# Kernel tuning notes

Measured on AMD Instinct MI355X. Metric: run time of the kernel, lower is better.

The kernel has to match this reference:

```python
import jax, jax.numpy as jnp
import numpy as np

B, H, W, C = 32, 64, 64, 256


def setup_inputs() -> dict:
    key = jax.random.key(0)
    kq, kk, kv = jax.random.split(key, 3)
    query = jax.random.normal(kq, (B, H, W, C), dtype=jnp.float32)
    keys = jax.random.normal(kk, (B, H, W, C), dtype=jnp.float32)
    values = jax.random.normal(kv, (B, H, W, C), dtype=jnp.float32)
    return {"query": query, "keys": keys, "values": values}


def reference(query, keys, values):
    # A[b,q,k] = sum_{h,w} query[b,h,w,q] * keys[b,h,w,k]
    scores = jnp.einsum("bhwq,bhwk->bqk", query, keys)
    attn = jax.nn.softmax(scores, axis=-1)  # softmax over keys axis
    # out[b,q,h,w] = sum_k attn[b,q,k] * values[b,h,w,k]
    out = jnp.einsum("bqk,bhwk->bqhw", attn, values)
    return out
```

## Files before the change

kernel.cpp:

```cpp
#include <hip/hip_runtime.h>
#include <hip/hip_bf16.h>

#define B_  32
#define HW_ 4096
#define C_  256

using bf16x8 = __attribute__((ext_vector_type(8))) short;
using f32x4  = __attribute__((ext_vector_type(4))) float;
using u32x4  = __attribute__((ext_vector_type(4))) uint;

__device__ __forceinline__ ushort f2bf_rn(float x) {
    uint u = __builtin_bit_cast(uint, x);
    u += 0x7FFFu + ((u >> 16) & 1u);
    return (ushort)(u >> 16);
}
__device__ __forceinline__ uint pk_bf2(float a, float b) {
    return ((uint)f2bf_rn(b) << 16) | (uint)f2bf_rn(a);
}
__device__ __forceinline__ uint pk_rtz(float x0, float x1) {
    return __builtin_amdgcn_perm(__builtin_bit_cast(uint, x1),
                                 __builtin_bit_cast(uint, x0), 0x07060302u);
}
__device__ __forceinline__ void split2_rtz(float x0, float x1, uint& hi2, uint& lo2) {
    uint u0 = __builtin_bit_cast(uint, x0), u1 = __builtin_bit_cast(uint, x1);
    hi2 = __builtin_amdgcn_perm(u1, u0, 0x07060302u);
    float h0 = __builtin_bit_cast(float, u0 & 0xFFFF0000u);
    float h1 = __builtin_bit_cast(float, u1 & 0xFFFF0000u);
    lo2 = pk_rtz(x0 - h0, x1 - h1);
}
__device__ __forceinline__ void frag_from_f32(const f32x4& f0, const f32x4& f1,
                                              bf16x8& hi, bf16x8& lo) {
    uint h0, l0, h1, l1, h2, l2, h3, l3;
    split2_rtz(f0[0], f0[1], h0, l0);
    split2_rtz(f0[2], f0[3], h1, l1);
    split2_rtz(f1[0], f1[1], h2, l2);
    split2_rtz(f1[2], f1[3], h3, l3);
    hi = __builtin_bit_cast(bf16x8, (u32x4){h0, h1, h2, h3});
    lo = __builtin_bit_cast(bf16x8, (u32x4){l0, l1, l2, l3});
}

__global__ __launch_bounds__(512, 4) void scores_kernel(const float* __restrict__ qg,
                                                        const float* __restrict__ kg,
                                                        float* __restrict__ scores) {
    int x  = blockIdx.x;
    int s  = x & 7;
    int tn = (x >> 3) & 1;
    int tm = (x >> 4) & 1;
    int b  = x >> 5;

    __shared__ __align__(16) float Qt[128 * 32], Kt[128 * 32];

    int tid = threadIdx.x, lane = tid & 63, w = tid >> 6;
    int m0 = (w >> 2) * 64;
    int n0 = (w & 3) * 32;
    int g = lane >> 4, r16 = lane & 15;

    int cc = tid & 127;
    int s0 = (tid >> 7) * 2;
    int hh = s0 * 4;

    int wi0 = cc * 32 + ((s0 ^ (cc & 7)) * 4);
    int wi1 = cc * 32 + (((s0 + 1) ^ (cc & 7)) * 4);

    const float* qcol = qg + (size_t)b * HW_ * C_ + tm * 128 + cc;
    const float* kcol = kg + (size_t)b * HW_ * C_ + tn * 128 + cc;

    f32x4 acc[4][2];
#pragma unroll
    for (int i = 0; i < 4; ++i)
#pragma unroll
        for (int j = 0; j < 2; ++j) acc[i][j] = (f32x4){0.f, 0.f, 0.f, 0.f};

#define LOAD_QK(qr, kr, itv) {                                                 \
        int hw0 = s * 512 + (itv) * 32 + hh;                                   \
        const float* qp = qcol + (size_t)hw0 * C_;                             \
        const float* kp = kcol + (size_t)hw0 * C_;                             \
        _Pragma("unroll")                                                      \
        for (int j = 0; j < 8; ++j) qr[j] = qp[(size_t)j * C_];                \
        _Pragma("unroll")                                                      \
        for (int j = 0; j < 8; ++j) kr[j] = kp[(size_t)j * C_];                \
    }

#define STORE_RAW(qr, kr) {                                                    \
        *reinterpret_cast<f32x4*>(&Qt[wi0]) = (f32x4){qr[0], qr[1], qr[2], qr[3]}; \
        *reinterpret_cast<f32x4*>(&Qt[wi1]) = (f32x4){qr[4], qr[5], qr[6], qr[7]}; \
        *reinterpret_cast<f32x4*>(&Kt[wi0]) = (f32x4){kr[0], kr[1], kr[2], kr[3]}; \
        *reinterpret_cast<f32x4*>(&Kt[wi1]) = (f32x4){kr[4], kr[5], kr[6], kr[7]}; \
    }

#define MFMA_PHASE() {                                                         \
        bf16x8 ahi[4], alo[4];                                                 \
        _Pragma("unroll")                                                      \
        for (int mi = 0; mi < 4; ++mi) {                                       \
            int row = m0 + mi * 16 + r16, key = row & 7;                       \
            f32x4 f0 = *reinterpret_cast<const f32x4*>(&Qt[row * 32 + (((2*g)   ^ key) * 4)]); \
            f32x4 f1 = *reinterpret_cast<const f32x4*>(&Qt[row * 32 + (((2*g+1) ^ key) * 4)]); \
            frag_from_f32(f0, f1, ahi[mi], alo[mi]);                           \
        }                                                                      \
        _Pragma("unroll")                                                      \
        for (int ni = 0; ni < 2; ++ni) {                                       \
            int row = n0 + ni * 16 + r16, key = row & 7;                       \
            f32x4 f0 = *reinterpret_cast<const f32x4*>(&Kt[row * 32 + (((2*g)   ^ key) * 4)]); \
            f32x4 f1 = *reinterpret_cast<const f32x4*>(&Kt[row * 32 + (((2*g+1) ^ key) * 4)]); \
            bf16x8 bhi, blo;                                                   \
            frag_from_f32(f0, f1, bhi, blo);                                   \
            _Pragma("unroll")                                                  \
            for (int mi = 0; mi < 4; ++mi) {                                   \
                acc[mi][ni] = __builtin_amdgcn_mfma_f32_16x16x32_bf16(ahi[mi], bhi, acc[mi][ni], 0, 0, 0); \
                acc[mi][ni] = __builtin_amdgcn_mfma_f32_16x16x32_bf16(ahi[mi], blo, acc[mi][ni], 0, 0, 0); \
                acc[mi][ni] = __builtin_amdgcn_mfma_f32_16x16x32_bf16(alo[mi], bhi, acc[mi][ni], 0, 0, 0); \
            }                                                                  \
        }                                                                      \
    }

#define STEP(qc, kc, qn, kn, itv, doload) {                                    \
        if (doload) LOAD_QK(qn, kn, (itv) + 1);                                \
        __syncthreads();                                                       \
        STORE_RAW(qc, kc);                                                     \
        __syncthreads();                                                       \
        MFMA_PHASE();                                                          \
    }

    float qa[8], ka[8], qb[8], kb[8];
    LOAD_QK(qa, ka, 0);
    for (int p = 0; p < 8; ++p) {
        STEP(qa, ka, qb, kb, 2 * p, true);
        STEP(qb, kb, qa, ka, 2 * p + 1, p < 7);
    }

#pragma unroll
    for (int mi = 0; mi < 4; ++mi)
#pragma unroll
        for (int ni = 0; ni < 2; ++ni)
#pragma unroll
            for (int r = 0; r < 4; ++r) {
                int qrow = tm * 128 + m0 + mi * 16 + g * 4 + r;
                int kc   = tn * 128 + n0 + ni * 16 + r16;
                atomicAdd(&scores[((size_t)b * 256 + qrow) * 256 + kc], acc[mi][ni][r]);
            }
#undef STEP
#undef MFMA_PHASE
#undef STORE_RAW
#undef LOAD_QK
}

__global__ __launch_bounds__(256) void softmax_kernel(const float* __restrict__ scores,
                                                      ushort* __restrict__ attn) {
    int wid  = blockIdx.x * 4 + (threadIdx.x >> 6);
    int lane = threadIdx.x & 63;
    const float4 v = *reinterpret_cast<const float4*>(scores + (size_t)wid * 256 + lane * 4);
    float m = fmaxf(fmaxf(v.x, v.y), fmaxf(v.z, v.w));
#pragma unroll
    for (int off = 32; off; off >>= 1) m = fmaxf(m, __shfl_xor(m, off, 64));
    float e0 = __expf(v.x - m), e1 = __expf(v.y - m), e2 = __expf(v.z - m), e3 = __expf(v.w - m);
    float ssum = e0 + e1 + e2 + e3;
#pragma unroll
    for (int off = 32; off; off >>= 1) ssum += __shfl_xor(ssum, off, 64);
    float inv = 1.0f / ssum;
    uint2 o;
    o.x = pk_bf2(e0 * inv, e1 * inv);
    o.y = pk_bf2(e2 * inv, e3 * inv);
    *reinterpret_cast<uint2*>(attn + (size_t)wid * 256 + lane * 4) = o;
}

__global__ __launch_bounds__(256, 4) void pv_kernel(const ushort* __restrict__ attn,
                                                    const float* __restrict__ vg,
                                                    float* __restrict__ out) {
    int b   = blockIdx.x >> 6;
    int hw0 = (blockIdx.x & 63) * 64;
    int tid = threadIdx.x, lane = tid & 63, w = tid >> 6;
    int m0  = w * 64;
    int g   = lane >> 4, r16 = lane & 15;

    __shared__ __align__(16) float Vt[2 * 64 * 32];

    int srow = tid >> 2;
    int sslot = (tid & 3) * 2;
    int wi0 = srow * 32 + ((sslot ^ (srow & 7)) * 4);
    int wi1 = srow * 32 + (((sslot + 1) ^ (srow & 7)) * 4);
    const float* vstage = vg + ((size_t)(b * HW_ + hw0 + srow)) * C_ + sslot * 4;

    const ushort* abase = attn + (size_t)b * 256 * 256 + g * 8;

    f32x4 acc[4][4];
#pragma unroll
    for (int i = 0; i < 4; ++i)
#pragma unroll
        for (int j = 0; j < 4; ++j) acc[i][j] = (f32x4){0.f, 0.f, 0.f, 0.f};

    {
        f32x4 p0 = *reinterpret_cast<const f32x4*>(vstage);
        f32x4 p1 = *reinterpret_cast<const f32x4*>(vstage + 4);
        *reinterpret_cast<f32x4*>(&Vt[wi0]) = p0;
        *reinterpret_cast<f32x4*>(&Vt[wi1]) = p1;
    }
    __syncthreads();

    for (int p = 0; p < 8; ++p) {
        float* rbuf = &Vt[(p & 1) * 64 * 32];
        float* wbuf = &Vt[((p + 1) & 1) * 64 * 32];

        f32x4 n0v, n1v;
        if (p < 7) {
            n0v = *reinterpret_cast<const f32x4*>(vstage + (p + 1) * 32);
            n1v = *reinterpret_cast<const f32x4*>(vstage + (p + 1) * 32 + 4);
        }

        int k0 = p * 32;
        bf16x8 a[4];
#pragma unroll
        for (int mi = 0; mi < 4; ++mi)
            a[mi] = *reinterpret_cast<const bf16x8*>(abase + (size_t)(m0 + mi * 16 + r16) * 256 + k0);

#pragma unroll
        for (int ni = 0; ni < 4; ++ni) {
            int row = ni * 16 + r16, key = row & 7;
            f32x4 f0 = *reinterpret_cast<const f32x4*>(&rbuf[row * 32 + (((2 * g)     ^ key) * 4)]);
            f32x4 f1 = *reinterpret_cast<const f32x4*>(&rbuf[row * 32 + (((2 * g + 1) ^ key) * 4)]);
            bf16x8 bf = __builtin_bit_cast(bf16x8, (u32x4){
                pk_rtz(f0[0], f0[1]), pk_rtz(f0[2], f0[3]),
                pk_rtz(f1[0], f1[1]), pk_rtz(f1[2], f1[3])});
#pragma unroll
            for (int mi = 0; mi < 4; ++mi)
                acc[mi][ni] = __builtin_amdgcn_mfma_f32_16x16x32_bf16(a[mi], bf, acc[mi][ni], 0, 0, 0);
        }

        if (p < 7) {
            *reinterpret_cast<f32x4*>(&wbuf[wi0]) = n0v;
            *reinterpret_cast<f32x4*>(&wbuf[wi1]) = n1v;
            __syncthreads();
        }
    }

#pragma unroll
    for (int mi = 0; mi < 4; ++mi)
#pragma unroll
        for (int ni = 0; ni < 4; ++ni)
#pragma unroll
            for (int r = 0; r < 4; ++r) {
                int qrow = m0 + mi * 16 + g * 4 + r;
                int hw   = hw0 + ni * 16 + r16;
                out[((size_t)b * 256 + qrow) * 4096 + hw] = acc[mi][ni][r];
            }
}

extern "C" void kernel_launch(void* const* d_in, const int* in_sizes, int n_in,
                              void* d_out, int out_size, void* d_ws, size_t ws_size,
                              hipStream_t stream) {
    const float* q = (const float*)d_in[0];
    const float* k = (const float*)d_in[1];
    const float* v = (const float*)d_in[2];
    float* out = (float*)d_out;

    float*  scores = (float*)d_ws;
    ushort* attn   = (ushort*)((char*)d_ws + (size_t)B_ * 256 * 256 * 4);

    (void)hipMemsetAsync(d_ws, 0, (size_t)B_ * 256 * 256 * 4, stream);
    scores_kernel<<<1024, 512, 0, stream>>>(q, k, scores);
    softmax_kernel<<<2048, 256, 0, stream>>>(scores, attn);
    pv_kernel<<<2048, 256, 0, stream>>>(attn, v, out);
}
```

Baseline: 185.9 us.

## Pre-split Q/K to bf16 hi/lo in LDS and enlarge per-wave tiles

The scores kernel now converts Q and K to bf16 hi/lo pairs once, when staging into padded LDS buffers. Previously every wave re-split fp32 values after reading them from LDS. Blocks shrink to 256 threads with 64x64 tiles per wave, which gives more MFMA reuse per fragment load. The register double-buffered prefetch is dropped in favour of a simple load-sync-store loop with raised wave priority around the MFMAs. Larger accumulators and more loads in flight per thread may raise register pressure, and without prefetch less load latency is hidden.

```diff
diff --git a/kernel.cpp b/kernel.cpp
--- a/kernel.cpp
+++ b/kernel.cpp
@@ -4,6 +4,7 @@
 #define B_  32
 #define HW_ 4096
 #define C_  256
+#define S_LDS 40
 
 using bf16x8 = __attribute__((ext_vector_type(8))) short;
 using f32x4  = __attribute__((ext_vector_type(4))) float;
@@ -28,18 +29,8 @@
     float h1 = __builtin_bit_cast(float, u1 & 0xFFFF0000u);
     lo2 = pk_rtz(x0 - h0, x1 - h1);
 }
-__device__ __forceinline__ void frag_from_f32(const f32x4& f0, const f32x4& f1,
-                                              bf16x8& hi, bf16x8& lo) {
-    uint h0, l0, h1, l1, h2, l2, h3, l3;
-    split2_rtz(f0[0], f0[1], h0, l0);
-    split2_rtz(f0[2], f0[3], h1, l1);
-    split2_rtz(f1[0], f1[1], h2, l2);
-    split2_rtz(f1[2], f1[3], h3, l3);
-    hi = __builtin_bit_cast(bf16x8, (u32x4){h0, h1, h2, h3});
-    lo = __builtin_bit_cast(bf16x8, (u32x4){l0, l1, l2, l3});
-}
-
-__global__ __launch_bounds__(512, 4) void scores_kernel(const float* __restrict__ qg,
+
+__global__ __launch_bounds__(256, 4) void scores_kernel(const float* __restrict__ qg,
                                                         const float* __restrict__ kg,
                                                         float* __restrict__ scores) {
     int x  = blockIdx.x;
@@ -48,100 +39,90 @@
     int tm = (x >> 4) & 1;
     int b  = x >> 5;
 
-    __shared__ __align__(16) float Qt[128 * 32], Kt[128 * 32];
+    __shared__ __align__(16) ushort Qhi[128 * S_LDS], Qlo[128 * S_LDS];
+    __shared__ __align__(16) ushort Khi[128 * S_LDS], Klo[128 * S_LDS];
 
     int tid = threadIdx.x, lane = tid & 63, w = tid >> 6;
-    int m0 = (w >> 2) * 64;
-    int n0 = (w & 3) * 32;
+    int m0 = (w >> 1) * 64;
+    int n0 = (w & 1) * 64;
     int g = lane >> 4, r16 = lane & 15;
 
-    int cc = tid & 127;
-    int s0 = (tid >> 7) * 2;
-    int hh = s0 * 4;
-
-    int wi0 = cc * 32 + ((s0 ^ (cc & 7)) * 4);
-    int wi1 = cc * 32 + (((s0 + 1) ^ (cc & 7)) * 4);
-
-    const float* qcol = qg + (size_t)b * HW_ * C_ + tm * 128 + cc;
-    const float* kcol = kg + (size_t)b * HW_ * C_ + tn * 128 + cc;
-
-    f32x4 acc[4][2];
+    int cq = tid & 127;
+    int hq = (tid >> 7) * 16;
+
+    const float* qcol = qg + (size_t)b * HW_ * C_ + tm * 128 + cq;
+    const float* kcol = kg + (size_t)b * HW_ * C_ + tn * 128 + cq;
+
+    f32x4 acc[4][4];
 #pragma unroll
     for (int i = 0; i < 4; ++i)
 #pragma unroll
-        for (int j = 0; j < 2; ++j) acc[i][j] = (f32x4){0.f, 0.f, 0.f, 0.f};
-
-#define LOAD_QK(qr, kr, itv) {                                                 \
-        int hw0 = s * 512 + (itv) * 32 + hh;                                   \
-        const float* qp = qcol + (size_t)hw0 * C_;                             \
-        const float* kp = kcol + (size_t)hw0 * C_;                             \
-        _Pragma("unroll")                                                      \
-        for (int j = 0; j < 8; ++j) qr[j] = qp[(size_t)j * C_];                \
-        _Pragma("unroll")                                                      \
-        for (int j = 0; j < 8; ++j) kr[j] = kp[(size_t)j * C_];                \
+        for (int j = 0; j < 4; ++j) acc[i][j] = (f32x4){0.f, 0.f, 0.f, 0.f};
+
+    for (int it = 0; it < 16; ++it) {
+        int hw0 = s * 512 + it * 32 + hq;
+
+        float qv[16], kv[16];
+        const float* qp = qcol + (size_t)hw0 * C_;
+        const float* kp = kcol + (size_t)hw0 * C_;
+#pragma unroll
+        for (int j = 0; j < 16; ++j) qv[j] = qp[(size_t)j * C_];
+#pragma unroll
+        for (int j = 0; j < 16; ++j) kv[j] = kp[(size_t)j * C_];
+
+        __syncthreads();
+
+        {
+            uint h[8], l[8];
+#pragma unroll
+            for (int p = 0; p < 8; ++p) split2_rtz(qv[2 * p], qv[2 * p + 1], h[p], l[p]);
+            int base = cq * S_LDS + hq;
+            *reinterpret_cast<u32x4*>(&Qhi[base])     = (u32x4){h[0], h[1], h[2], h[3]};
+            *reinterpret_cast<u32x4*>(&Qhi[base + 8]) = (u32x4){h[4], h[5], h[6], h[7]};
+            *reinterpret_cast<u32x4*>(&Qlo[base])     = (u32x4){l[0], l[1], l[2], l[3]};
+            *reinterpret_cast<u32x4*>(&Qlo[base + 8]) = (u32x4){l[4], l[5], l[6], l[7]};
+#pragma unroll
+            for (int p = 0; p < 8; ++p) split2_rtz(kv[2 * p], kv[2 * p + 1], h[p], l[p]);
+            *reinterpret_cast<u32x4*>(&Khi[base])     = (u32x4){h[0], h[1], h[2], h[3]};
+            *reinterpret_cast<u32x4*>(&Khi[base + 8]) = (u32x4){h[4], h[5], h[6], h[7]};
+            *reinterpret_cast<u32x4*>(&Klo[base])     = (u32x4){l[0], l[1], l[2], l[3]};
+            *reinterpret_cast<u32x4*>(&Klo[base + 8]) = (u32x4){l[4], l[5], l[6], l[7]};
+        }
+        __syncthreads();
+
+        __builtin_amdgcn_s_setprio(1);
+        bf16x8 ahi[4], alo[4];
+#pragma unroll
+        for (int mi = 0; mi < 4; ++mi) {
+            int off = (m0 + mi * 16 + r16) * S_LDS + g * 8;
+            ahi[mi] = *reinterpret_cast<const bf16x8*>(&Qhi[off]);
+            alo[mi] = *reinterpret_cast<const bf16x8*>(&Qlo[off]);
+        }
+#pragma unroll
+        for (int ni = 0; ni < 4; ++ni) {
+            int off = (n0 + ni * 16 + r16) * S_LDS + g * 8;
+            bf16x8 bhi = *reinterpret_cast<const bf16x8*>(&Khi[off]);
+            bf16x8 blo = *reinterpret_cast<const bf16x8*>(&Klo[off]);
+#pragma unroll
+            for (int mi = 0; mi < 4; ++mi) {
+                acc[mi][ni] = __builtin_amdgcn_mfma_f32_16x16x32_bf16(ahi[mi], bhi, acc[mi][ni], 0, 0, 0);
+                acc[mi][ni] = __builtin_amdgcn_mfma_f32_16x16x32_bf16(ahi[mi], blo, acc[mi][ni], 0, 0, 0);
+                acc[mi][ni] = __builtin_amdgcn_mfma_f32_16x16x32_bf16(alo[mi], bhi, acc[mi][ni], 0, 0, 0);
+            }
+        }
+        __builtin_amdgcn_s_setprio(0);
     }
 
-#define STORE_RAW(qr, kr) {                                                    \
-        *reinterpret_cast<f32x4*>(&Qt[wi0]) = (f32x4){qr[0], qr[1], qr[2], qr[3]}; \
-        *reinterpret_cast<f32x4*>(&Qt[wi1]) = (f32x4){qr[4], qr[5], qr[6], qr[7]}; \
-        *reinterpret_cast<f32x4*>(&Kt[wi0]) = (f32x4){kr[0], kr[1], kr[2], kr[3]}; \
-        *reinterpret_cast<f32x4*>(&Kt[wi1]) = (f32x4){kr[4], kr[5], kr[6], kr[7]}; \
-    }
-
-#define MFMA_PHASE() {                                                         \
-        bf16x8 ahi[4], alo[4];                                                 \
-        _Pragma("unroll")                                                      \
-        for (int mi = 0; mi < 4; ++mi) {                                       \
-            int row = m0 + mi * 16 + r16, key = row & 7;                       \
-            f32x4 f0 = *reinterpret_cast<const f32x4*>(&Qt[row * 32 + (((2*g)   ^ key) * 4)]); \
-            f32x4 f1 = *reinterpret_cast<const f32x4*>(&Qt[row * 32 + (((2*g+1) ^ key) * 4)]); \
-            frag_from_f32(f0, f1, ahi[mi], alo[mi]);                           \
-        }                                                                      \
-        _Pragma("unroll")                                                      \
-        for (int ni = 0; ni < 2; ++ni) {                                       \
-            int row = n0 + ni * 16 + r16, key = row & 7;                       \
-            f32x4 f0 = *reinterpret_cast<const f32x4*>(&Kt[row * 32 + (((2*g)   ^ key) * 4)]); \
-            f32x4 f1 = *reinterpret_cast<const f32x4*>(&Kt[row * 32 + (((2*g+1) ^ key) * 4)]); \
-            bf16x8 bhi, blo;                                                   \
-            frag_from_f32(f0, f1, bhi, blo);                                   \
-            _Pragma("unroll")                                                  \
-            for (int mi = 0; mi < 4; ++mi) {                                   \
-                acc[mi][ni] = __builtin_amdgcn_mfma_f32_16x16x32_bf16(ahi[mi], bhi, acc[mi][ni], 0, 0, 0); \
-                acc[mi][ni] = __builtin_amdgcn_mfma_f32_16x16x32_bf16(ahi[mi], blo, acc[mi][ni], 0, 0, 0); \
-                acc[mi][ni] = __builtin_amdgcn_mfma_f32_16x16x32_bf16(alo[mi], bhi, acc[mi][ni], 0, 0, 0); \
-            }                                                                  \
-        }                                                                      \
-    }
-
-#define STEP(qc, kc, qn, kn, itv, doload) {                                    \
-        if (doload) LOAD_QK(qn, kn, (itv) + 1);                                \
-        __syncthreads();                                                       \
-        STORE_RAW(qc, kc);                                                     \
-        __syncthreads();                                                       \
-        MFMA_PHASE();                                                          \
-    }
-
-    float qa[8], ka[8], qb[8], kb[8];
-    LOAD_QK(qa, ka, 0);
-    for (int p = 0; p < 8; ++p) {
-        STEP(qa, ka, qb, kb, 2 * p, true);
-        STEP(qb, kb, qa, ka, 2 * p + 1, p < 7);
-    }
-
 #pragma unroll
     for (int mi = 0; mi < 4; ++mi)
 #pragma unroll
-        for (int ni = 0; ni < 2; ++ni)
+        for (int ni = 0; ni < 4; ++ni)
 #pragma unroll
             for (int r = 0; r < 4; ++r) {
                 int qrow = tm * 128 + m0 + mi * 16 + g * 4 + r;
                 int kc   = tn * 128 + n0 + ni * 16 + r16;
                 atomicAdd(&scores[((size_t)b * 256 + qrow) * 256 + kc], acc[mi][ni][r]);
             }
-#undef STEP
-#undef MFMA_PHASE
-#undef STORE_RAW
-#undef LOAD_QK
 }
 
 __global__ __launch_bounds__(256) void softmax_kernel(const float* __restrict__ scores,
@@ -256,7 +237,7 @@
     ushort* attn   = (ushort*)((char*)d_ws + (size_t)B_ * 256 * 256 * 4);
 
     (void)hipMemsetAsync(d_ws, 0, (size_t)B_ * 256 * 256 * 4, stream);
-    scores_kernel<<<1024, 512, 0, stream>>>(q, k, scores);
+    scores_kernel<<<1024, 256, 0, stream>>>(q, k, scores);
     softmax_kernel<<<2048, 256, 0, stream>>>(scores, attn);
     pv_kernel<<<2048, 256, 0, stream>>>(attn, v, out);
 }
```

Result: slower. 193.2 us (+3.9%).

## Pre-split Q/K into bf16 hi/lo in LDS with double buffering, larger warp tiles

Applied to the files above, without the earlier changes.

The scores kernel now converts each fp32 Q/K element to bf16 hi/lo once, at store time, rather than every wave redoing the split from fp32 LDS reads. The LDS tiles are double-buffered with padded stride 72, which cuts the loop to one barrier per iteration. Blocks shrink from 512 to 256 threads, and each wave computes a 64x64 tile (4x4 MFMA accumulators) for more operand reuse. s_setprio is raised around the MFMA phase. This trades more registers per thread and lower occupancy for less redundant conversion and fewer syncs.

```diff
diff --git a/kernel.cpp b/kernel.cpp
--- a/kernel.cpp
+++ b/kernel.cpp
@@ -4,6 +4,8 @@
 #define B_  32
 #define HW_ 4096
 #define C_  256
+#define S72 72
+#define BUF_ (128 * S72)
 
 using bf16x8 = __attribute__((ext_vector_type(8))) short;
 using f32x4  = __attribute__((ext_vector_type(4))) float;
@@ -28,18 +30,8 @@
     float h1 = __builtin_bit_cast(float, u1 & 0xFFFF0000u);
     lo2 = pk_rtz(x0 - h0, x1 - h1);
 }
-__device__ __forceinline__ void frag_from_f32(const f32x4& f0, const f32x4& f1,
-                                              bf16x8& hi, bf16x8& lo) {
-    uint h0, l0, h1, l1, h2, l2, h3, l3;
-    split2_rtz(f0[0], f0[1], h0, l0);
-    split2_rtz(f0[2], f0[3], h1, l1);
-    split2_rtz(f1[0], f1[1], h2, l2);
-    split2_rtz(f1[2], f1[3], h3, l3);
-    hi = __builtin_bit_cast(bf16x8, (u32x4){h0, h1, h2, h3});
-    lo = __builtin_bit_cast(bf16x8, (u32x4){l0, l1, l2, l3});
-}
-
-__global__ __launch_bounds__(512, 4) void scores_kernel(const float* __restrict__ qg,
+
+__global__ __launch_bounds__(256, 2) void scores_kernel(const float* __restrict__ qg,
                                                         const float* __restrict__ kg,
                                                         float* __restrict__ scores) {
     int x  = blockIdx.x;
@@ -48,62 +40,68 @@
     int tm = (x >> 4) & 1;
     int b  = x >> 5;
 
-    __shared__ __align__(16) float Qt[128 * 32], Kt[128 * 32];
+    __shared__ __align__(16) ushort QHL[2 * BUF_], KHL[2 * BUF_];
 
     int tid = threadIdx.x, lane = tid & 63, w = tid >> 6;
-    int m0 = (w >> 2) * 64;
-    int n0 = (w & 3) * 32;
+    int m0 = (w >> 1) * 64;
+    int n0 = (w & 1) * 64;
     int g = lane >> 4, r16 = lane & 15;
 
     int cc = tid & 127;
-    int s0 = (tid >> 7) * 2;
-    int hh = s0 * 4;
-
-    int wi0 = cc * 32 + ((s0 ^ (cc & 7)) * 4);
-    int wi1 = cc * 32 + (((s0 + 1) ^ (cc & 7)) * 4);
+    int hh = (tid >> 7) * 16;
 
     const float* qcol = qg + (size_t)b * HW_ * C_ + tm * 128 + cc;
     const float* kcol = kg + (size_t)b * HW_ * C_ + tn * 128 + cc;
 
-    f32x4 acc[4][2];
+    f32x4 acc[4][4];
 #pragma unroll
     for (int i = 0; i < 4; ++i)
 #pragma unroll
-        for (int j = 0; j < 2; ++j) acc[i][j] = (f32x4){0.f, 0.f, 0.f, 0.f};
-
-#define LOAD_QK(qr, kr, itv) {                                                 \
+        for (int j = 0; j < 4; ++j) acc[i][j] = (f32x4){0.f, 0.f, 0.f, 0.f};
+
+    float qv[16], kv[16];
+
+#define LOAD_QK(itv) {                                                         \
         int hw0 = s * 512 + (itv) * 32 + hh;                                   \
         const float* qp = qcol + (size_t)hw0 * C_;                             \
         const float* kp = kcol + (size_t)hw0 * C_;                             \
         _Pragma("unroll")                                                      \
-        for (int j = 0; j < 8; ++j) qr[j] = qp[(size_t)j * C_];                \
-        _Pragma("unroll")                                                      \
-        for (int j = 0; j < 8; ++j) kr[j] = kp[(size_t)j * C_];                \
-    }
-
-#define STORE_RAW(qr, kr) {                                                    \
-        *reinterpret_cast<f32x4*>(&Qt[wi0]) = (f32x4){qr[0], qr[1], qr[2], qr[3]}; \
-        *reinterpret_cast<f32x4*>(&Qt[wi1]) = (f32x4){qr[4], qr[5], qr[6], qr[7]}; \
-        *reinterpret_cast<f32x4*>(&Kt[wi0]) = (f32x4){kr[0], kr[1], kr[2], kr[3]}; \
-        *reinterpret_cast<f32x4*>(&Kt[wi1]) = (f32x4){kr[4], kr[5], kr[6], kr[7]}; \
-    }
-
-#define MFMA_PHASE() {                                                         \
+        for (int j = 0; j < 16; ++j) qv[j] = qp[(size_t)j * C_];               \
+        _Pragma("unroll")                                                      \
+        for (int j = 0; j < 16; ++j) kv[j] = kp[(size_t)j * C_];               \
+    }
+
+#define CONVERT_STORE(ofs) {                                                   \
+        uint h[8], l[8];                                                       \
+        _Pragma("unroll")                                                      \
+        for (int p = 0; p < 8; ++p) split2_rtz(qv[2 * p], qv[2 * p + 1], h[p], l[p]); \
+        int bh = (ofs) + cc * S72 + hh;                                        \
+        *reinterpret_cast<u32x4*>(&QHL[bh])      = (u32x4){h[0], h[1], h[2], h[3]}; \
+        *reinterpret_cast<u32x4*>(&QHL[bh + 8])  = (u32x4){h[4], h[5], h[6], h[7]}; \
+        *reinterpret_cast<u32x4*>(&QHL[bh + 32]) = (u32x4){l[0], l[1], l[2], l[3]}; \
+        *reinterpret_cast<u32x4*>(&QHL[bh + 40]) = (u32x4){l[4], l[5], l[6], l[7]}; \
+        _Pragma("unroll")                                                      \
+        for (int p = 0; p < 8; ++p) split2_rtz(kv[2 * p], kv[2 * p + 1], h[p], l[p]); \
+        *reinterpret_cast<u32x4*>(&KHL[bh])      = (u32x4){h[0], h[1], h[2], h[3]}; \
+        *reinterpret_cast<u32x4*>(&KHL[bh + 8])  = (u32x4){h[4], h[5], h[6], h[7]}; \
+        *reinterpret_cast<u32x4*>(&KHL[bh + 32]) = (u32x4){l[0], l[1], l[2], l[3]}; \
+        *reinterpret_cast<u32x4*>(&KHL[bh + 40]) = (u32x4){l[4], l[5], l[6], l[7]}; \
+    }
+
+#define MFMA_PHASE(ofs) {                                                      \
+        __builtin_amdgcn_s_setprio(1);                                         \
         bf16x8 ahi[4], alo[4];                                                 \
         _Pragma("unroll")                                                      \
         for (int mi = 0; mi < 4; ++mi) {                                       \
-            int row = m0 + mi * 16 + r16, key = row & 7;                       \
-            f32x4 f0 = *reinterpret_cast<const f32x4*>(&Qt[row * 32 + (((2*g)   ^ key) * 4)]); \
-            f32x4 f1 = *reinterpret_cast<const f32x4*>(&Qt[row * 32 + (((2*g+1) ^ key) * 4)]); \
-            frag_from_f32(f0, f1, ahi[mi], alo[mi]);                           \
+            int ro = (ofs) + (m0 + mi * 16 + r16) * S72 + g * 8;               \
+            ahi[mi] = *reinterpret_cast<const bf16x8*>(&QHL[ro]);              \
+            alo[mi] = *reinterpret_cast<const bf16x8*>(&QHL[ro + 32]);         \
         }                                                                      \
         _Pragma("unroll")                                                      \
-        for (int ni = 0; ni < 2; ++ni) {                                       \
-            int row = n0 + ni * 16 + r16, key = row & 7;                       \
-            f32x4 f0 = *reinterpret_cast<const f32x4*>(&Kt[row * 32 + (((2*g)   ^ key) * 4)]); \
-            f32x4 f1 = *reinterpret_cast<const f32x4*>(&Kt[row * 32 + (((2*g+1) ^ key) * 4)]); \
-            bf16x8 bhi, blo;                                                   \
-            frag_from_f32(f0, f1, bhi, blo);                                   \
+        for (int ni = 0; ni < 4; ++ni) {                                       \
+            int ro = (ofs) + (n0 + ni * 16 + r16) * S72 + g * 8;               \
+            bf16x8 bhi = *reinterpret_cast<const bf16x8*>(&KHL[ro]);           \
+            bf16x8 blo = *reinterpret_cast<const bf16x8*>(&KHL[ro + 32]);      \
             _Pragma("unroll")                                                  \
             for (int mi = 0; mi < 4; ++mi) {                                   \
                 acc[mi][ni] = __builtin_amdgcn_mfma_f32_16x16x32_bf16(ahi[mi], bhi, acc[mi][ni], 0, 0, 0); \
@@ -111,36 +109,37 @@
                 acc[mi][ni] = __builtin_amdgcn_mfma_f32_16x16x32_bf16(alo[mi], bhi, acc[mi][ni], 0, 0, 0); \
             }                                                                  \
         }                                                                      \
-    }
-
-#define STEP(qc, kc, qn, kn, itv, doload) {                                    \
-        if (doload) LOAD_QK(qn, kn, (itv) + 1);                                \
-        __syncthreads();                                                       \
-        STORE_RAW(qc, kc);                                                     \
-        __syncthreads();                                                       \
-        MFMA_PHASE();                                                          \
-    }
-
-    float qa[8], ka[8], qb[8], kb[8];
-    LOAD_QK(qa, ka, 0);
-    for (int p = 0; p < 8; ++p) {
-        STEP(qa, ka, qb, kb, 2 * p, true);
-        STEP(qb, kb, qa, ka, 2 * p + 1, p < 7);
+        __builtin_amdgcn_s_setprio(0);                                         \
+    }
+
+    LOAD_QK(0);
+    CONVERT_STORE(0);
+    __syncthreads();
+
+#pragma unroll 2
+    for (int it = 0; it < 16; ++it) {
+        int cofs = (it & 1) * BUF_;
+        int nofs = ((it + 1) & 1) * BUF_;
+        if (it < 15) LOAD_QK(it + 1);
+        MFMA_PHASE(cofs);
+        if (it < 15) {
+            CONVERT_STORE(nofs);
+            __syncthreads();
+        }
     }
 
 #pragma unroll
     for (int mi = 0; mi < 4; ++mi)
 #pragma unroll
-        for (int ni = 0; ni < 2; ++ni)
+        for (int ni = 0; ni < 4; ++ni)
 #pragma unroll
             for (int r = 0; r < 4; ++r) {
                 int qrow = tm * 128 + m0 + mi * 16 + g * 4 + r;
                 int kc   = tn * 128 + n0 + ni * 16 + r16;
                 atomicAdd(&scores[((size_t)b * 256 + qrow) * 256 + kc], acc[mi][ni][r]);
             }
-#undef STEP
 #undef MFMA_PHASE
-#undef STORE_RAW
+#undef CONVERT_STORE
 #undef LOAD_QK
 }
 
@@ -256,7 +255,7 @@
     ushort* attn   = (ushort*)((char*)d_ws + (size_t)B_ * 256 * 256 * 4);
 
     (void)hipMemsetAsync(d_ws, 0, (size_t)B_ * 256 * 256 * 4, stream);
-    scores_kernel<<<1024, 512, 0, stream>>>(q, k, scores);
+    scores_kernel<<<1024, 256, 0, stream>>>(q, k, scores);
     softmax_kernel<<<2048, 256, 0, stream>>>(scores, attn);
     pv_kernel<<<2048, 256, 0, stream>>>(attn, v, out);
 }
```

After: 193.8 us. +4.2%, slower.
